# Performance work log

Measured on AMD Instinct MI355X. Metric: run time of the kernel, lower is better.

The kernel has to match this reference:

```python
import jax, jax.numpy as jnp
import numpy as np

D_MODEL = 1024
NHEAD = 16
HEAD_DIM = D_MODEL // NHEAD
B, T = 2, 2048


def setup_inputs() -> dict:
    key = jax.random.key(0)
    ks = jax.random.split(key, 12)
    s = 1.0 / np.sqrt(D_MODEL)
    return {
        "query": jax.random.normal(ks[0], (B, T, D_MODEL), jnp.float32),
        "key": jax.random.normal(ks[1], (B, T, D_MODEL), jnp.float32),
        "value": jax.random.normal(ks[2], (B, T, D_MODEL), jnp.float32),
        "key_padding_mask": jnp.zeros((B, T), dtype=bool),
        "attn_mask": jnp.zeros((T, T), jnp.float32),
        "stoich_frac": jax.random.uniform(ks[3], (B, T), jnp.float32),
        "Wq": jax.random.uniform(ks[4], (D_MODEL, D_MODEL), jnp.float32, -s, s),
        "bq": jnp.zeros((D_MODEL,), jnp.float32),
        "Wk": jax.random.uniform(ks[5], (D_MODEL, D_MODEL), jnp.float32, -s, s),
        "bk": jnp.zeros((D_MODEL,), jnp.float32),
        "Wv": jax.random.uniform(ks[6], (D_MODEL, D_MODEL), jnp.float32, -s, s),
        "bv": jnp.zeros((D_MODEL,), jnp.float32),
        "Wo": jax.random.uniform(ks[7], (D_MODEL, D_MODEL), jnp.float32, -s, s),
        "bo": jnp.zeros((D_MODEL,), jnp.float32),
        "stoich_alpha": jnp.float32(0.1),
    }


def reference(query, key, value, key_padding_mask, attn_mask, stoich_frac,
              Wq, bq, Wk, bk, Wv, bv, Wo, bo, stoich_alpha):
    Bq, Tq, _ = query.shape
    Tk = key.shape[1]
    scale = HEAD_DIM ** -0.5
    # Linear projections (torch Linear: x @ W.T + b), reshape to [B, H, T, Dh]
    Q = (query @ Wq.T + bq).reshape(Bq, Tq, NHEAD, HEAD_DIM).transpose(0, 2, 1, 3)
    K = (key @ Wk.T + bk).reshape(Bq, Tk, NHEAD, HEAD_DIM).transpose(0, 2, 1, 3)
    V = (value @ Wv.T + bv).reshape(Bq, Tk, NHEAD, HEAD_DIM).transpose(0, 2, 1, 3)
    # Scores [B, H, Tq, Tk]
    scores = jnp.einsum("bhqd,bhkd->bhqk", Q, K) * scale
    # Stoichiometric pairwise bias (T_q == T_k path)
    diff = stoich_frac[:, :, None] - stoich_frac[:, None, :]  # [B, Tq, Tk]
    bias = stoich_alpha * (jnp.log1p(jnp.abs(diff)) * jnp.sign(diff))
    scores = scores + bias[:, None, :, :]
    scores = scores + attn_mask  # broadcasts [Tq, Tk]
    scores = jnp.where(key_padding_mask[:, None, None, :], -jnp.inf, scores)
    probs = jax.nn.softmax(scores, axis=-1)
    # dropout: eval mode / p=0 -> identity
    out = jnp.einsum("bhqk,bhkd->bhqd", probs, V)
    out = out.transpose(0, 2, 1, 3).reshape(Bq, Tq, D_MODEL)
    return out @ Wo.T + bo
```

## Files before the change

### kernel.cpp

```cpp
#include <hip/hip_runtime.h>
#include <math.h>

typedef __bf16 bf16_t;
typedef __bf16 bf16x8 __attribute__((ext_vector_type(8)));
typedef __bf16 bf16x4 __attribute__((ext_vector_type(4)));
typedef float  f32x4  __attribute__((ext_vector_type(4)));

#define NHEAD 16
#define HDIM 64
#define DMODEL 1024
#define TSEQ 2048

__device__ __forceinline__ f32x4 mfma16(bf16x8 a, bf16x8 b, f32x4 c) {
  return __builtin_amdgcn_mfma_f32_16x16x32_bf16(a, b, c, 0, 0, 0);
}

__device__ __forceinline__ void gload16(const bf16_t* g, bf16_t* l) {
  __builtin_amdgcn_global_load_lds((const __attribute__((address_space(1))) void*)g,
                                   (__attribute__((address_space(3))) void*)l, 16, 0, 0);
}

__device__ __forceinline__ unsigned pk2(float lo, float hi) {
  unsigned short a = __builtin_bit_cast(unsigned short, (__bf16)lo);
  unsigned short c = __builtin_bit_cast(unsigned short, (__bf16)hi);
  return ((unsigned)c << 16) | a;
}

__device__ __forceinline__ void cvtstore(f32x4 x0, f32x4 x1, bf16_t* dh, bf16_t* dl, int off) {
  bf16x8 hfr, lfr;
#pragma unroll
  for (int j = 0; j < 4; ++j) {
    float v = x0[j];
    __bf16 hb = (__bf16)v;
    hfr[j] = hb; lfr[j] = (__bf16)(v - (float)hb);
    float w = x1[j];
    __bf16 wb = (__bf16)w;
    hfr[4 + j] = wb; lfr[4 + j] = (__bf16)(w - (float)wb);
  }
  *(bf16x8*)(dh + off) = hfr;
  *(bf16x8*)(dl + off) = lfr;
}

__global__ __launch_bounds__(256)
void build_bias(const float* __restrict__ amask, const unsigned char* __restrict__ kpm,
                const float* __restrict__ sf, const float* __restrict__ alpha_p,
                bf16_t* __restrict__ BM) {
  size_t idx = (size_t)blockIdx.x * 256 + threadIdx.x;
  int k8 = (int)(idx & (TSEQ / 8 - 1));
  size_t bq = idx >> 8;
  int b = (int)(bq >> 11);
  int q = (int)(bq & (TSEQ - 1));
  const float sfq = sf[bq];
  const float alpha = *alpha_p;
  const float* sfk = sf + (size_t)b * TSEQ + k8 * 8;
  const float* am  = amask + (size_t)q * TSEQ + k8 * 8;
  const unsigned char* kp = kpm + (size_t)b * TSEQ + k8 * 8;
  bf16x8 o;
#pragma unroll
  for (int j = 0; j < 8; ++j) {
    float df = sfq - sfk[j];
    float v = alpha * copysignf(log1pf(fabsf(df)), df) + am[j];
    if (kp[j]) v = -1.0e30f;
    o[j] = (__bf16)v;
  }
  *(bf16x8*)&BM[idx * 8] = o;
}

template<int MODE>
__global__ __launch_bounds__(256)
void gemm_mfma(const float* __restrict__ A, const float* __restrict__ W,
               const float* __restrict__ bias,
               bf16_t* __restrict__ obh, bf16_t* __restrict__ obl,
               float* __restrict__ of) {
  __shared__ bf16_t AH[8 * 512], AL[8 * 512], WH[4 * 512], WL[4 * 512];
  const int tid = threadIdx.x;
  const int lane = tid & 63;
  const int a15 = lane & 15, g = lane >> 4;
  const int wv = tid >> 6, wm = wv >> 1, wn = wv & 1;
  const int m0 = blockIdx.y * 128, n0 = blockIdx.x * 64;
  constexpr int NI = (MODE == 2) ? 2 : 4;
  constexpr int NJ = (MODE == 2) ? 4 : 2;
  f32x4 acc[NI][NJ] = {};

  const int s0 = tid, s1 = tid + 256;
  const int t0 = s0 >> 6, l0 = s0 & 63;
  const int t1 = s1 >> 6, l1 = s1 & 63;
  const float* pA0 = A + (size_t)(m0 + t0 * 16 + (l0 & 15)) * DMODEL + 8 * (l0 >> 4);
  const float* pA1 = A + (size_t)(m0 + t1 * 16 + (l1 & 15)) * DMODEL + 8 * (l1 >> 4);
  const float* pW  = W + (size_t)(n0 + t0 * 16 + (l0 & 15)) * DMODEL + 8 * (l0 >> 4);

  f32x4 rA0a = *(const f32x4*)pA0, rA0b = *(const f32x4*)(pA0 + 4);
  f32x4 rA1a = *(const f32x4*)pA1, rA1b = *(const f32x4*)(pA1 + 4);
  f32x4 rWa  = *(const f32x4*)pW,  rWb  = *(const f32x4*)(pW + 4);

  for (int k0 = 0; k0 < DMODEL; k0 += 32) {
    __syncthreads();
    cvtstore(rA0a, rA0b, AH, AL, s0 * 8);
    cvtstore(rA1a, rA1b, AH, AL, s1 * 8);
    cvtstore(rWa,  rWb,  WH, WL, s0 * 8);
    if (k0 + 32 < DMODEL) {
      pA0 += 32; pA1 += 32; pW += 32;
      rA0a = *(const f32x4*)pA0; rA0b = *(const f32x4*)(pA0 + 4);
      rA1a = *(const f32x4*)pA1; rA1b = *(const f32x4*)(pA1 + 4);
      rWa  = *(const f32x4*)pW;  rWb  = *(const f32x4*)(pW + 4);
    }
    __syncthreads();

    bf16x8 ah[4], al[4], wh[2], wl[2];
#pragma unroll
    for (int i = 0; i < 4; ++i) {
      ah[i] = *(const bf16x8*)&AH[(wm * 4 + i) * 512 + lane * 8];
      al[i] = *(const bf16x8*)&AL[(wm * 4 + i) * 512 + lane * 8];
    }
#pragma unroll
    for (int j = 0; j < 2; ++j) {
      wh[j] = *(const bf16x8*)&WH[(wn * 2 + j) * 512 + lane * 8];
      wl[j] = *(const bf16x8*)&WL[(wn * 2 + j) * 512 + lane * 8];
    }
    if (MODE == 2) {
#pragma unroll
      for (int i = 0; i < 2; ++i)
#pragma unroll
        for (int j = 0; j < 4; ++j) {
          acc[i][j] = mfma16(wh[i], ah[j], acc[i][j]);
          acc[i][j] = mfma16(wh[i], al[j], acc[i][j]);
          acc[i][j] = mfma16(wl[i], ah[j], acc[i][j]);
        }
    } else {
#pragma unroll
      for (int i = 0; i < 4; ++i)
#pragma unroll
        for (int j = 0; j < 2; ++j) {
          acc[i][j] = mfma16(ah[i], wh[j], acc[i][j]);
          acc[i][j] = mfma16(ah[i], wl[j], acc[i][j]);
          acc[i][j] = mfma16(al[i], wh[j], acc[i][j]);
        }
    }
  }

  if (MODE == 0) {
#pragma unroll
    for (int i = 0; i < 4; ++i)
#pragma unroll
      for (int j = 0; j < 2; ++j) {
        int n = n0 + wn * 32 + j * 16 + a15;
        float bs = bias[n];
#pragma unroll
        for (int r = 0; r < 4; ++r) {
          int m = m0 + wm * 64 + i * 16 + 4 * g + r;
          of[(size_t)m * DMODEL + n] = acc[i][j][r] + bs;
        }
      }
  } else if (MODE == 1) {
#pragma unroll
    for (int i = 0; i < 4; ++i)
#pragma unroll
      for (int j = 0; j < 2; ++j) {
        int n = n0 + wn * 32 + j * 16 + a15;
        float bs = bias[n];
        int hh = n >> 6, d = n & 63;
#pragma unroll
        for (int r = 0; r < 4; ++r) {
          int m = m0 + wm * 64 + i * 16 + 4 * g + r;
          int bb = m >> 11, t = m & (TSEQ - 1);
          float v = acc[i][j][r] + bs;
          size_t o = (((size_t)(bb * NHEAD + hh)) * TSEQ + t) * HDIM + d;
          __bf16 hb = (__bf16)v;
          obh[o] = hb;
          obl[o] = (__bf16)(v - (float)hb);
        }
      }
  } else {
#pragma unroll
    for (int i = 0; i < 2; ++i)
#pragma unroll
      for (int j = 0; j < 4; ++j) {
        int m = m0 + wm * 64 + j * 16 + a15;
        int bb = m >> 11, t = m & (TSEQ - 1);
#pragma unroll
        for (int r = 0; r < 4; ++r) {
          int n = n0 + wn * 32 + i * 16 + 4 * g + r;
          float v = acc[i][j][r] + bias[n];
          int hh = n >> 6, d = n & 63;
          size_t o = (((size_t)(bb * NHEAD + hh)) * HDIM + d) * TSEQ + t;
          __bf16 hb = (__bf16)v;
          obh[o] = hb;
          obl[o] = (__bf16)(v - (float)hb);
        }
      }
  }
}

__global__ __launch_bounds__(256)
void attn_mfma(const bf16_t* __restrict__ Qhi, const bf16_t* __restrict__ Qlo,
               const bf16_t* __restrict__ Khi, const bf16_t* __restrict__ Klo,
               const bf16_t* __restrict__ Vth, const bf16_t* __restrict__ Vtl,
               const bf16_t* __restrict__ BMt, float* __restrict__ O) {
  __shared__ bf16_t KH[2][8 * 512], KL[2][8 * 512], VH[2][8 * 512], VL[2][8 * 512];
  const int tid = threadIdx.x;
  const int lane = tid & 63, wv = tid >> 6;
  const int a15 = lane & 15, g = lane >> 4;
  const int b = blockIdx.z, h = blockIdx.y, q0 = blockIdx.x * 64;
  const int bh = b * NHEAD + h;
  const int qg = q0 + wv * 16 + a15;

  const bf16_t* Qh_b = Qhi + ((size_t)bh * TSEQ + qg) * HDIM;
  const bf16_t* Ql_b = Qlo + ((size_t)bh * TSEQ + qg) * HDIM;
  const bf16_t* Kh_b = Khi + (size_t)bh * TSEQ * HDIM;
  const bf16_t* Kl_b = Klo + (size_t)bh * TSEQ * HDIM;
  const bf16_t* Vh_b = Vth + (size_t)bh * HDIM * TSEQ;
  const bf16_t* Vl_b = Vtl + (size_t)bh * HDIM * TSEQ;
  const bf16_t* bmrow = BMt + ((size_t)b * TSEQ + qg) * TSEQ;

  bf16x8 qh[2], ql[2];
  qh[0] = *(const bf16x8*)&Qh_b[8 * g];
  qh[1] = *(const bf16x8*)&Qh_b[32 + 8 * g];
  ql[0] = *(const bf16x8*)&Ql_b[8 * g];
  ql[1] = *(const bf16x8*)&Ql_b[32 + 8 * g];

  f32x4 aco[4] = {};
  float m_run = -3.0e38f, l_run = 0.f;

  auto stage = [&](int k0, int buf) {
#pragma unroll
    for (int c = 0; c < 2; ++c) {
      int sb = wv * 2 + c;
      int ts = sb >> 1, ks = sb & 1;
      size_t ko = (size_t)(k0 + 16 * ts + a15) * HDIM + 32 * ks + 8 * g;
      gload16(Kh_b + ko, &KH[buf][sb * 512]);
      gload16(Kl_b + ko, &KL[buf][sb * 512]);
      size_t vo = (size_t)(16 * ts + a15) * TSEQ + k0 + 32 * ks + 8 * g;
      gload16(Vh_b + vo, &VH[buf][sb * 512]);
      gload16(Vl_b + vo, &VL[buf][sb * 512]);
    }
  };

  stage(0, 0);
  __syncthreads();

  for (int t = 0; t < TSEQ / 64; ++t) {
    const int k0 = t * 64;
    const int cur = t & 1;
    if (t + 1 < TSEQ / 64) stage(k0 + 64, cur ^ 1);

    bf16x4 bmv[4];
#pragma unroll
    for (int mt = 0; mt < 4; ++mt) bmv[mt] = *(const bf16x4*)&bmrow[k0 + 16 * mt + 4 * g];

    f32x4 s4[4];
    __builtin_amdgcn_s_setprio(1);
#pragma unroll
    for (int mt = 0; mt < 4; ++mt) {
      bf16x8 k0h = *(const bf16x8*)&KH[cur][(mt * 2 + 0) * 512 + lane * 8];
      bf16x8 k1h = *(const bf16x8*)&KH[cur][(mt * 2 + 1) * 512 + lane * 8];
      bf16x8 k0l = *(const bf16x8*)&KL[cur][(mt * 2 + 0) * 512 + lane * 8];
      bf16x8 k1l = *(const bf16x8*)&KL[cur][(mt * 2 + 1) * 512 + lane * 8];
      f32x4 sa = {};
      sa = mfma16(k0h, qh[0], sa);
      sa = mfma16(k1h, qh[1], sa);
      sa = mfma16(k0h, ql[0], sa);
      sa = mfma16(k1h, ql[1], sa);
      sa = mfma16(k0l, qh[0], sa);
      sa = mfma16(k1l, qh[1], sa);
      s4[mt] = sa;
    }
    __builtin_amdgcn_s_setprio(0);

#pragma unroll
    for (int mt = 0; mt < 4; ++mt)
#pragma unroll
      for (int r = 0; r < 4; ++r)
        s4[mt][r] = fmaf(s4[mt][r], 0.125f, (float)bmv[mt][r]);

    float tmax = -3.0e38f;
#pragma unroll
    for (int mt = 0; mt < 4; ++mt)
#pragma unroll
      for (int r = 0; r < 4; ++r) tmax = fmaxf(tmax, s4[mt][r]);
    tmax = fmaxf(tmax, __shfl_xor(tmax, 16));
    tmax = fmaxf(tmax, __shfl_xor(tmax, 32));
    float mnew = fmaxf(m_run, tmax);
    float corr = __expf(m_run - mnew);
    float psum = 0.f;
    unsigned pk01[4], pk23[4];
#pragma unroll
    for (int mt = 0; mt < 4; ++mt) {
      float p0 = __expf(s4[mt][0] - mnew);
      float p1 = __expf(s4[mt][1] - mnew);
      float p2 = __expf(s4[mt][2] - mnew);
      float p3 = __expf(s4[mt][3] - mnew);
      psum += (p0 + p1) + (p2 + p3);
      pk01[mt] = pk2(p0, p1);
      pk23[mt] = pk2(p2, p3);
    }
    psum += __shfl_xor(psum, 16);
    psum += __shfl_xor(psum, 32);
    l_run = l_run * corr + psum;
    m_run = mnew;
#pragma unroll
    for (int dt = 0; dt < 4; ++dt) aco[dt] *= corr;

    bf16x8 pf[2];
#pragma unroll
    for (int ks = 0; ks < 2; ++ks) {
      int src0 = a15 + 16 * (2 * (g & 1));
      int src1 = src0 + 16;
      unsigned A0 = __shfl(pk01[2 * ks + 0], src0), A1 = __shfl(pk01[2 * ks + 1], src0);
      unsigned B0 = __shfl(pk23[2 * ks + 0], src0), B1 = __shfl(pk23[2 * ks + 1], src0);
      unsigned C0 = __shfl(pk01[2 * ks + 0], src1), C1 = __shfl(pk01[2 * ks + 1], src1);
      unsigned D0 = __shfl(pk23[2 * ks + 0], src1), D1 = __shfl(pk23[2 * ks + 1], src1);
      bool hi2 = (g >> 1) & 1;
      uint4 wds;
      wds.x = hi2 ? A1 : A0;
      wds.y = hi2 ? B1 : B0;
      wds.z = hi2 ? C1 : C0;
      wds.w = hi2 ? D1 : D0;
      pf[ks] = __builtin_bit_cast(bf16x8, wds);
    }

    __builtin_amdgcn_s_setprio(1);
#pragma unroll
    for (int dt = 0; dt < 4; ++dt) {
#pragma unroll
      for (int ks = 0; ks < 2; ++ks) {
        bf16x8 vh = *(const bf16x8*)&VH[cur][(dt * 2 + ks) * 512 + lane * 8];
        bf16x8 vl = *(const bf16x8*)&VL[cur][(dt * 2 + ks) * 512 + lane * 8];
        aco[dt] = mfma16(vh, pf[ks], aco[dt]);
        aco[dt] = mfma16(vl, pf[ks], aco[dt]);
      }
    }
    __builtin_amdgcn_s_setprio(0);

    __syncthreads();
  }

  float inv = 1.0f / l_run;
#pragma unroll
  for (int dt = 0; dt < 4; ++dt) {
    f32x4 o = aco[dt] * inv;
    *(f32x4*)&O[((size_t)b * TSEQ + qg) * DMODEL + h * HDIM + dt * 16 + 4 * g] = o;
  }
}

extern "C" void kernel_launch(void* const* d_in, const int* in_sizes, int n_in,
                              void* d_out, int out_size, void* d_ws, size_t ws_size,
                              hipStream_t stream) {
  const float* query = (const float*)d_in[0];
  const float* key = (const float*)d_in[1];
  const float* value = (const float*)d_in[2];
  const unsigned char* kpm = (const unsigned char*)d_in[3];
  const float* amask = (const float*)d_in[4];
  const float* sf = (const float*)d_in[5];
  const float* Wq = (const float*)d_in[6];
  const float* bq = (const float*)d_in[7];
  const float* Wk = (const float*)d_in[8];
  const float* bk = (const float*)d_in[9];
  const float* Wv = (const float*)d_in[10];
  const float* bv = (const float*)d_in[11];
  const float* Wo = (const float*)d_in[12];
  const float* bo = (const float*)d_in[13];
  const float* alpha = (const float*)d_in[14];
  float* out = (float*)d_out;

  const size_t NEL = (size_t)2 * NHEAD * TSEQ * HDIM;
  bf16_t* p = (bf16_t*)d_ws;
  bf16_t* Qh = p;
  bf16_t* Ql = p + NEL;
  bf16_t* Kh = p + 2 * NEL;
  bf16_t* Kl = p + 3 * NEL;
  bf16_t* Vh = p + 4 * NEL;
  bf16_t* Vl = p + 5 * NEL;
  float* Oa = (float*)(p + 6 * NEL);
  bf16_t* BMt = (bf16_t*)(Oa + (size_t)4096 * DMODEL);

  dim3 bb(256);
  build_bias<<<dim3(4096), bb, 0, stream>>>(amask, kpm, sf, alpha, BMt);

  dim3 gg(16, 32);
  gemm_mfma<1><<<gg, bb, 0, stream>>>(query, Wq, bq, Qh, Ql, nullptr);
  gemm_mfma<1><<<gg, bb, 0, stream>>>(key, Wk, bk, Kh, Kl, nullptr);
  gemm_mfma<2><<<gg, bb, 0, stream>>>(value, Wv, bv, Vh, Vl, nullptr);
  dim3 ga(TSEQ / 64, NHEAD, 2);
  attn_mfma<<<ga, bb, 0, stream>>>(Qh, Ql, Kh, Kl, Vh, Vl, BMt, Oa);
  gemm_mfma<0><<<gg, bb, 0, stream>>>(Oa, Wo, bo, nullptr, nullptr, out);
}
```

Measured before the change: 398.0 us.

## Stage attention K/V through registers with single LDS buffer and lazy rescale

```diff
diff --git a/kernel.cpp b/kernel.cpp
--- a/kernel.cpp
+++ b/kernel.cpp
@@ -11,13 +11,12 @@
 #define DMODEL 1024
 #define TSEQ 2048
 
+#define LGKM0() do { asm volatile("s_waitcnt lgkmcnt(0)" ::: "memory"); \
+                     __builtin_amdgcn_sched_barrier(0); } while (0)
+#define SBAR() __builtin_amdgcn_s_barrier()
+
 __device__ __forceinline__ f32x4 mfma16(bf16x8 a, bf16x8 b, f32x4 c) {
   return __builtin_amdgcn_mfma_f32_16x16x32_bf16(a, b, c, 0, 0, 0);
-}
-
-__device__ __forceinline__ void gload16(const bf16_t* g, bf16_t* l) {
-  __builtin_amdgcn_global_load_lds((const __attribute__((address_space(1))) void*)g,
-                                   (__attribute__((address_space(3))) void*)l, 16, 0, 0);
 }
 
 __device__ __forceinline__ unsigned pk2(float lo, float hi) {
@@ -94,17 +93,19 @@
   f32x4 rWa  = *(const f32x4*)pW,  rWb  = *(const f32x4*)(pW + 4);
 
   for (int k0 = 0; k0 < DMODEL; k0 += 32) {
-    __syncthreads();
+    SBAR();
     cvtstore(rA0a, rA0b, AH, AL, s0 * 8);
     cvtstore(rA1a, rA1b, AH, AL, s1 * 8);
     cvtstore(rWa,  rWb,  WH, WL, s0 * 8);
+    __builtin_amdgcn_sched_barrier(0);
     if (k0 + 32 < DMODEL) {
       pA0 += 32; pA1 += 32; pW += 32;
       rA0a = *(const f32x4*)pA0; rA0b = *(const f32x4*)(pA0 + 4);
       rA1a = *(const f32x4*)pA1; rA1b = *(const f32x4*)(pA1 + 4);
       rWa  = *(const f32x4*)pW;  rWb  = *(const f32x4*)(pW + 4);
     }
-    __syncthreads();
+    LGKM0();
+    SBAR();
 
     bf16x8 ah[4], al[4], wh[2], wl[2];
 #pragma unroll
@@ -117,6 +118,7 @@
       wh[j] = *(const bf16x8*)&WH[(wn * 2 + j) * 512 + lane * 8];
       wl[j] = *(const bf16x8*)&WL[(wn * 2 + j) * 512 + lane * 8];
     }
+    __builtin_amdgcn_s_setprio(1);
     if (MODE == 2) {
 #pragma unroll
       for (int i = 0; i < 2; ++i)
@@ -136,6 +138,7 @@
           acc[i][j] = mfma16(al[i], wh[j], acc[i][j]);
         }
     }
+    __builtin_amdgcn_s_setprio(0);
   }
 
   if (MODE == 0) {
@@ -191,25 +194,26 @@
   }
 }
 
-__global__ __launch_bounds__(256)
+__global__ __launch_bounds__(256, 4)
 void attn_mfma(const bf16_t* __restrict__ Qhi, const bf16_t* __restrict__ Qlo,
                const bf16_t* __restrict__ Khi, const bf16_t* __restrict__ Klo,
                const bf16_t* __restrict__ Vth, const bf16_t* __restrict__ Vtl,
                const bf16_t* __restrict__ BMt, float* __restrict__ O) {
-  __shared__ bf16_t KH[2][8 * 512], KL[2][8 * 512], VH[2][8 * 512], VL[2][8 * 512];
+  __shared__ bf16_t KH[8 * 512], KL[8 * 512], VH[8 * 512], VL[8 * 512];
   const int tid = threadIdx.x;
   const int lane = tid & 63, wv = tid >> 6;
   const int a15 = lane & 15, g = lane >> 4;
   const int b = blockIdx.z, h = blockIdx.y, q0 = blockIdx.x * 64;
   const int bh = b * NHEAD + h;
   const int qg = q0 + wv * 16 + a15;
+  constexpr int NT = TSEQ / 64;
 
   const bf16_t* Qh_b = Qhi + ((size_t)bh * TSEQ + qg) * HDIM;
   const bf16_t* Ql_b = Qlo + ((size_t)bh * TSEQ + qg) * HDIM;
-  const bf16_t* Kh_b = Khi + (size_t)bh * TSEQ * HDIM;
-  const bf16_t* Kl_b = Klo + (size_t)bh * TSEQ * HDIM;
-  const bf16_t* Vh_b = Vth + (size_t)bh * HDIM * TSEQ;
-  const bf16_t* Vl_b = Vtl + (size_t)bh * HDIM * TSEQ;
+  const bf16_t* Kh_s = Khi + (size_t)bh * TSEQ * HDIM + (size_t)(16 * wv + a15) * HDIM + 8 * g;
+  const bf16_t* Kl_s = Klo + (size_t)bh * TSEQ * HDIM + (size_t)(16 * wv + a15) * HDIM + 8 * g;
+  const bf16_t* Vh_s = Vth + (size_t)bh * HDIM * TSEQ + (size_t)(16 * wv + a15) * TSEQ + 8 * g;
+  const bf16_t* Vl_s = Vtl + (size_t)bh * HDIM * TSEQ + (size_t)(16 * wv + a15) * TSEQ + 8 * g;
   const bf16_t* bmrow = BMt + ((size_t)b * TSEQ + qg) * TSEQ;
 
   bf16x8 qh[2], ql[2];
@@ -221,40 +225,50 @@
   f32x4 aco[4] = {};
   float m_run = -3.0e38f, l_run = 0.f;
 
-  auto stage = [&](int k0, int buf) {
+  uint4 rg[8];
+  bf16x4 bmv[4], bmn[4];
+
+#pragma unroll
+  for (int mt = 0; mt < 4; ++mt) bmv[mt] = *(const bf16x4*)&bmrow[16 * mt + 4 * g];
+#pragma unroll
+  for (int c = 0; c < 2; ++c) {
+    rg[0 + c] = *(const uint4*)(Kh_s + 32 * c);
+    rg[2 + c] = *(const uint4*)(Kl_s + 32 * c);
+    rg[4 + c] = *(const uint4*)(Vh_s + 32 * c);
+    rg[6 + c] = *(const uint4*)(Vl_s + 32 * c);
+  }
+
+  for (int t = 0; t < NT; ++t) {
 #pragma unroll
     for (int c = 0; c < 2; ++c) {
       int sb = wv * 2 + c;
-      int ts = sb >> 1, ks = sb & 1;
-      size_t ko = (size_t)(k0 + 16 * ts + a15) * HDIM + 32 * ks + 8 * g;
-      gload16(Kh_b + ko, &KH[buf][sb * 512]);
-      gload16(Kl_b + ko, &KL[buf][sb * 512]);
-      size_t vo = (size_t)(16 * ts + a15) * TSEQ + k0 + 32 * ks + 8 * g;
-      gload16(Vh_b + vo, &VH[buf][sb * 512]);
-      gload16(Vl_b + vo, &VL[buf][sb * 512]);
-    }
-  };
-
-  stage(0, 0);
-  __syncthreads();
-
-  for (int t = 0; t < TSEQ / 64; ++t) {
-    const int k0 = t * 64;
-    const int cur = t & 1;
-    if (t + 1 < TSEQ / 64) stage(k0 + 64, cur ^ 1);
-
-    bf16x4 bmv[4];
-#pragma unroll
-    for (int mt = 0; mt < 4; ++mt) bmv[mt] = *(const bf16x4*)&bmrow[k0 + 16 * mt + 4 * g];
+      *(uint4*)&KH[sb * 512 + lane * 8] = rg[0 + c];
+      *(uint4*)&KL[sb * 512 + lane * 8] = rg[2 + c];
+      *(uint4*)&VH[sb * 512 + lane * 8] = rg[4 + c];
+      *(uint4*)&VL[sb * 512 + lane * 8] = rg[6 + c];
+    }
+    __builtin_amdgcn_sched_barrier(0);
+    const int kn = (t + 1) * 64;
+    if (t + 1 < NT) {
+#pragma unroll
+      for (int mt = 0; mt < 4; ++mt) bmn[mt] = *(const bf16x4*)&bmrow[kn + 16 * mt + 4 * g];
+#pragma unroll
+      for (int c = 0; c < 2; ++c) {
+        rg[0 + c] = *(const uint4*)(Kh_s + (size_t)kn * HDIM + 32 * c);
+        rg[2 + c] = *(const uint4*)(Kl_s + (size_t)kn * HDIM + 32 * c);
+      }
+    }
+    LGKM0();
+    SBAR();
 
     f32x4 s4[4];
     __builtin_amdgcn_s_setprio(1);
 #pragma unroll
     for (int mt = 0; mt < 4; ++mt) {
-      bf16x8 k0h = *(const bf16x8*)&KH[cur][(mt * 2 + 0) * 512 + lane * 8];
-      bf16x8 k1h = *(const bf16x8*)&KH[cur][(mt * 2 + 1) * 512 + lane * 8];
-      bf16x8 k0l = *(const bf16x8*)&KL[cur][(mt * 2 + 0) * 512 + lane * 8];
-      bf16x8 k1l = *(const bf16x8*)&KL[cur][(mt * 2 + 1) * 512 + lane * 8];
+      bf16x8 k0h = *(const bf16x8*)&KH[(mt * 2 + 0) * 512 + lane * 8];
+      bf16x8 k1h = *(const bf16x8*)&KH[(mt * 2 + 1) * 512 + lane * 8];
+      bf16x8 k0l = *(const bf16x8*)&KL[(mt * 2 + 0) * 512 + lane * 8];
+      bf16x8 k1l = *(const bf16x8*)&KL[(mt * 2 + 1) * 512 + lane * 8];
       f32x4 sa = {};
       sa = mfma16(k0h, qh[0], sa);
       sa = mfma16(k1h, qh[1], sa);
@@ -265,6 +279,14 @@
       s4[mt] = sa;
     }
     __builtin_amdgcn_s_setprio(0);
+    __builtin_amdgcn_sched_barrier(0);
+    if (t + 1 < NT) {
+#pragma unroll
+      for (int c = 0; c < 2; ++c) {
+        rg[4 + c] = *(const uint4*)(Vh_s + kn + 32 * c);
+        rg[6 + c] = *(const uint4*)(Vl_s + kn + 32 * c);
+      }
+    }
 
 #pragma unroll
     for (int mt = 0; mt < 4; ++mt)
@@ -279,26 +301,29 @@
       for (int r = 0; r < 4; ++r) tmax = fmaxf(tmax, s4[mt][r]);
     tmax = fmaxf(tmax, __shfl_xor(tmax, 16));
     tmax = fmaxf(tmax, __shfl_xor(tmax, 32));
-    float mnew = fmaxf(m_run, tmax);
-    float corr = __expf(m_run - mnew);
+    if (!__all(tmax - m_run <= 8.0f)) {
+      float mnew = fmaxf(m_run, tmax);
+      float corr = __expf(m_run - mnew);
+      l_run *= corr;
+#pragma unroll
+      for (int dt = 0; dt < 4; ++dt) aco[dt] *= corr;
+      m_run = mnew;
+    }
     float psum = 0.f;
     unsigned pk01[4], pk23[4];
 #pragma unroll
     for (int mt = 0; mt < 4; ++mt) {
-      float p0 = __expf(s4[mt][0] - mnew);
-      float p1 = __expf(s4[mt][1] - mnew);
-      float p2 = __expf(s4[mt][2] - mnew);
-      float p3 = __expf(s4[mt][3] - mnew);
+      float p0 = __expf(s4[mt][0] - m_run);
+      float p1 = __expf(s4[mt][1] - m_run);
+      float p2 = __expf(s4[mt][2] - m_run);
+      float p3 = __expf(s4[mt][3] - m_run);
       psum += (p0 + p1) + (p2 + p3);
       pk01[mt] = pk2(p0, p1);
       pk23[mt] = pk2(p2, p3);
     }
     psum += __shfl_xor(psum, 16);
     psum += __shfl_xor(psum, 32);
-    l_run = l_run * corr + psum;
-    m_run = mnew;
-#pragma unroll
-    for (int dt = 0; dt < 4; ++dt) aco[dt] *= corr;
+    l_run += psum;
 
     bf16x8 pf[2];
 #pragma unroll
@@ -323,15 +348,19 @@
     for (int dt = 0; dt < 4; ++dt) {
 #pragma unroll
       for (int ks = 0; ks < 2; ++ks) {
-        bf16x8 vh = *(const bf16x8*)&VH[cur][(dt * 2 + ks) * 512 + lane * 8];
-        bf16x8 vl = *(const bf16x8*)&VL[cur][(dt * 2 + ks) * 512 + lane * 8];
+        bf16x8 vh = *(const bf16x8*)&VH[(dt * 2 + ks) * 512 + lane * 8];
+        bf16x8 vl = *(const bf16x8*)&VL[(dt * 2 + ks) * 512 + lane * 8];
         aco[dt] = mfma16(vh, pf[ks], aco[dt]);
         aco[dt] = mfma16(vl, pf[ks], aco[dt]);
       }
     }
     __builtin_amdgcn_s_setprio(0);
 
-    __syncthreads();
+    if (t + 1 < NT) {
+#pragma unroll
+      for (int mt = 0; mt < 4; ++mt) bmv[mt] = bmn[mt];
+    }
+    SBAR();
   }
 
   float inv = 1.0f / l_run;
```

Result: slower. 579.4 us (+45.6%).

## Replace syncthreads with explicit waitcnt barriers, prefetch bias, lazy softmax rescale

Applied to the files above, without the earlier changes.

```diff
diff --git a/kernel.cpp b/kernel.cpp
--- a/kernel.cpp
+++ b/kernel.cpp
@@ -10,6 +10,10 @@
 #define HDIM 64
 #define DMODEL 1024
 #define TSEQ 2048
+
+#define SBAR() __builtin_amdgcn_s_barrier()
+#define LGKM0() do { asm volatile("s_waitcnt lgkmcnt(0)" ::: "memory"); \
+                     __builtin_amdgcn_sched_barrier(0); } while (0)
 
 __device__ __forceinline__ f32x4 mfma16(bf16x8 a, bf16x8 b, f32x4 c) {
   return __builtin_amdgcn_mfma_f32_16x16x32_bf16(a, b, c, 0, 0, 0);
@@ -94,17 +98,19 @@
   f32x4 rWa  = *(const f32x4*)pW,  rWb  = *(const f32x4*)(pW + 4);
 
   for (int k0 = 0; k0 < DMODEL; k0 += 32) {
-    __syncthreads();
+    SBAR();
     cvtstore(rA0a, rA0b, AH, AL, s0 * 8);
     cvtstore(rA1a, rA1b, AH, AL, s1 * 8);
     cvtstore(rWa,  rWb,  WH, WL, s0 * 8);
+    __builtin_amdgcn_sched_barrier(0);
     if (k0 + 32 < DMODEL) {
       pA0 += 32; pA1 += 32; pW += 32;
       rA0a = *(const f32x4*)pA0; rA0b = *(const f32x4*)(pA0 + 4);
       rA1a = *(const f32x4*)pA1; rA1b = *(const f32x4*)(pA1 + 4);
       rWa  = *(const f32x4*)pW;  rWb  = *(const f32x4*)(pW + 4);
     }
-    __syncthreads();
+    LGKM0();
+    SBAR();
 
     bf16x8 ah[4], al[4], wh[2], wl[2];
 #pragma unroll
@@ -117,6 +123,7 @@
       wh[j] = *(const bf16x8*)&WH[(wn * 2 + j) * 512 + lane * 8];
       wl[j] = *(const bf16x8*)&WL[(wn * 2 + j) * 512 + lane * 8];
     }
+    __builtin_amdgcn_s_setprio(1);
     if (MODE == 2) {
 #pragma unroll
       for (int i = 0; i < 2; ++i)
@@ -136,6 +143,7 @@
           acc[i][j] = mfma16(al[i], wh[j], acc[i][j]);
         }
     }
+    __builtin_amdgcn_s_setprio(0);
   }
 
   if (MODE == 0) {
@@ -203,6 +211,7 @@
   const int b = blockIdx.z, h = blockIdx.y, q0 = blockIdx.x * 64;
   const int bh = b * NHEAD + h;
   const int qg = q0 + wv * 16 + a15;
+  constexpr int NT = TSEQ / 64;
 
   const bf16_t* Qh_b = Qhi + ((size_t)bh * TSEQ + qg) * HDIM;
   const bf16_t* Ql_b = Qlo + ((size_t)bh * TSEQ + qg) * HDIM;
@@ -220,32 +229,38 @@
 
   f32x4 aco[4] = {};
   float m_run = -3.0e38f, l_run = 0.f;
+  bf16x4 bmv[4], bmn[4];
 
   auto stage = [&](int k0, int buf) {
 #pragma unroll
     for (int c = 0; c < 2; ++c) {
       int sb = wv * 2 + c;
-      int ts = sb >> 1, ks = sb & 1;
-      size_t ko = (size_t)(k0 + 16 * ts + a15) * HDIM + 32 * ks + 8 * g;
+      size_t ko = (size_t)(k0 + 16 * wv + a15) * HDIM + 32 * c + 8 * g;
       gload16(Kh_b + ko, &KH[buf][sb * 512]);
       gload16(Kl_b + ko, &KL[buf][sb * 512]);
-      size_t vo = (size_t)(16 * ts + a15) * TSEQ + k0 + 32 * ks + 8 * g;
+      size_t vo = (size_t)(16 * wv + a15) * TSEQ + k0 + 32 * c + 8 * g;
       gload16(Vh_b + vo, &VH[buf][sb * 512]);
       gload16(Vl_b + vo, &VL[buf][sb * 512]);
     }
   };
 
+#pragma unroll
+  for (int mt = 0; mt < 4; ++mt) bmv[mt] = *(const bf16x4*)&bmrow[16 * mt + 4 * g];
   stage(0, 0);
-  __syncthreads();
-
-  for (int t = 0; t < TSEQ / 64; ++t) {
-    const int k0 = t * 64;
+
+  for (int t = 0; t < NT; ++t) {
     const int cur = t & 1;
-    if (t + 1 < TSEQ / 64) stage(k0 + 64, cur ^ 1);
-
-    bf16x4 bmv[4];
-#pragma unroll
-    for (int mt = 0; mt < 4; ++mt) bmv[mt] = *(const bf16x4*)&bmrow[k0 + 16 * mt + 4 * g];
+    if (t + 1 < NT) {
+      const int kn = (t + 1) * 64;
+#pragma unroll
+      for (int mt = 0; mt < 4; ++mt) bmn[mt] = *(const bf16x4*)&bmrow[kn + 16 * mt + 4 * g];
+      stage(kn, cur ^ 1);
+      asm volatile("s_waitcnt vmcnt(12)" ::: "memory");
+    } else {
+      asm volatile("s_waitcnt vmcnt(0)" ::: "memory");
+    }
+    __builtin_amdgcn_sched_barrier(0);
+    SBAR();
 
     f32x4 s4[4];
     __builtin_amdgcn_s_setprio(1);
@@ -279,26 +294,29 @@
       for (int r = 0; r < 4; ++r) tmax = fmaxf(tmax, s4[mt][r]);
     tmax = fmaxf(tmax, __shfl_xor(tmax, 16));
     tmax = fmaxf(tmax, __shfl_xor(tmax, 32));
-    float mnew = fmaxf(m_run, tmax);
-    float corr = __expf(m_run - mnew);
+    if (!__all(tmax - m_run <= 8.0f)) {
+      float mnew = fmaxf(m_run, tmax);
+      float corr = __expf(m_run - mnew);
+      l_run *= corr;
+#pragma unroll
+      for (int dt = 0; dt < 4; ++dt) aco[dt] *= corr;
+      m_run = mnew;
+    }
     float psum = 0.f;
     unsigned pk01[4], pk23[4];
 #pragma unroll
     for (int mt = 0; mt < 4; ++mt) {
-      float p0 = __expf(s4[mt][0] - mnew);
-      float p1 = __expf(s4[mt][1] - mnew);
-      float p2 = __expf(s4[mt][2] - mnew);
-      float p3 = __expf(s4[mt][3] - mnew);
+      float p0 = __expf(s4[mt][0] - m_run);
+      float p1 = __expf(s4[mt][1] - m_run);
+      float p2 = __expf(s4[mt][2] - m_run);
+      float p3 = __expf(s4[mt][3] - m_run);
       psum += (p0 + p1) + (p2 + p3);
       pk01[mt] = pk2(p0, p1);
       pk23[mt] = pk2(p2, p3);
     }
     psum += __shfl_xor(psum, 16);
     psum += __shfl_xor(psum, 32);
-    l_run = l_run * corr + psum;
-    m_run = mnew;
-#pragma unroll
-    for (int dt = 0; dt < 4; ++dt) aco[dt] *= corr;
+    l_run += psum;
 
     bf16x8 pf[2];
 #pragma unroll
@@ -331,7 +349,11 @@
     }
     __builtin_amdgcn_s_setprio(0);
 
-    __syncthreads();
+    if (t + 1 < NT) {
+#pragma unroll
+      for (int mt = 0; mt < 4; ++mt) bmv[mt] = bmn[mt];
+    }
+    SBAR();
   }
 
   float inv = 1.0f / l_run;
```

Result: no change. 400.1 us (+0.5%).
